# Optimization experiments

Measured on AMD Instinct MI355X. Metric: run time of the kernel, lower is better.

Reference implementation:

```python
import jax, jax.numpy as jnp
import numpy as np

NUM_COMPONENTS = 4
HEADS = 24
DIM_HEAD = 64
EPS = 1e-8

def setup_inputs() -> dict:
    key = jax.random.key(0)
    ks = jax.random.split(key, 6)
    BC, S, D = 8, 4096, 1536   # batch*components, spatial tokens, hidden dim
    T = 154                     # encoder (text) sequence length
    w_scale = D ** -0.5
    return {
        "hidden_states": jax.random.normal(ks[0], (BC, S, D), jnp.float32),
        "encoder_hidden_states": jax.random.normal(ks[1], (BC, T, D), jnp.float32),
        "Wq": jax.random.normal(ks[2], (D, D), jnp.float32) * w_scale,
        "bq": jnp.zeros((D,), jnp.float32),
        "Wk": jax.random.normal(ks[3], (D, D), jnp.float32) * w_scale,
        "bk": jnp.zeros((D,), jnp.float32),
        "Wv": jax.random.normal(ks[4], (D, D), jnp.float32) * w_scale,
        "bv": jnp.zeros((D,), jnp.float32),
        "Wo": jax.random.normal(ks[5], (D, D), jnp.float32) * w_scale,
        "bo": jnp.zeros((D,), jnp.float32),
    }

def reference(hidden_states, encoder_hidden_states, Wq, bq, Wk, bk, Wv, bv, Wo, bo):
    BC, S, D = hidden_states.shape
    T = encoder_hidden_states.shape[1]
    C = NUM_COMPONENTS
    B = BC // C
    H, dh = HEADS, DIM_HEAD
    scale = dh ** -0.5

    # linear projections (torch Linear: x @ W.T + b)
    q = hidden_states @ Wq.T + bq            # [BC, S, D]
    k = encoder_hidden_states @ Wk.T + bk     # [BC, T, D]
    v = encoder_hidden_states @ Wv.T + bv     # [BC, T, D]

    q = q.reshape(BC, S, H, dh).transpose(0, 2, 1, 3)  # [BC, H, S, dh]
    k = k.reshape(BC, T, H, dh).transpose(0, 2, 1, 3)  # [BC, H, T, dh]
    v = v.reshape(BC, T, H, dh).transpose(0, 2, 1, 3)  # [BC, H, T, dh]

    # full score tensor, softmax over the COMPONENT axis, then renormalize over keys
    scores = jnp.einsum('bhsd,bhtd->bhst', q, k) * scale        # [BC, H, S, T]
    scores = scores.reshape(C, B, H, S, T)
    w = jax.nn.softmax(scores, axis=0).reshape(BC, H, S, T)
    w = w / (jnp.sum(w, axis=-1, keepdims=True) + EPS)

    out = jnp.einsum('bhst,bhtd->bhsd', w, v)                   # [BC, H, S, dh]
    out = out.transpose(0, 2, 1, 3).reshape(BC, S, D)
    out = out @ Wo.T + bo
    return out
```

## Files before the change

kernel.cpp:

```cpp
#include <hip/hip_runtime.h>


typedef unsigned short u16;
typedef unsigned int   u32;

#define NHS   50331648ULL
#define NEHS  1892352ULL
#define NW    2359296ULL
#define NVT   1966080ULL

using bf16x8 = __attribute__((ext_vector_type(8))) short;
using f32x4  = __attribute__((ext_vector_type(4))) float;

__device__ __forceinline__ u16 f2bf(float f) {
  union { float f; u32 u; } x{f};
  u32 r = (x.u + 0x7fffu + ((x.u >> 16) & 1u)) >> 16;
  return (u16)r;
}

__device__ __forceinline__ void gload_lds16(const u16* g, u16* s) {
  __builtin_amdgcn_global_load_lds((const __attribute__((address_space(1))) void*)g,
                                   (__attribute__((address_space(3))) void*)s,
                                   16, 0, 0);
}

__global__ void cvt_bf16(const float* __restrict__ src, u16* __restrict__ dst, int n4) {
  int idx = blockIdx.x * blockDim.x + threadIdx.x;
  int stride = gridDim.x * blockDim.x;
  for (int i = idx; i < n4; i += stride) {
    float4 v = ((const float4*)src)[i];
    ushort4 o;
    o.x = f2bf(v.x); o.y = f2bf(v.y); o.z = f2bf(v.z); o.w = f2bf(v.w);
    ((ushort4*)dst)[i] = o;
  }
}

template <int MODE>
__global__ __launch_bounds__(256)
void gemm_bt(const u16* __restrict__ A, const u16* __restrict__ Bw,
             const float* __restrict__ bias, void* __restrict__ Cv,
             int M, int K) {
  const int N = 1536;
  __shared__ __align__(16) u16 As[4096];
  __shared__ __align__(16) u16 Bs[4096];
  const int tid  = threadIdx.x;
  const int wv   = tid >> 6;
  const int lane = tid & 63;
  const int wr = wv >> 1, wc = wv & 1;
  const int l16 = lane & 15, quad = lane >> 4;
  const int m0 = blockIdx.y * 128, n0 = blockIdx.x * 128;
  const int r = tid >> 2, c8 = (tid & 3) * 8;

  int ra0 = m0 + r;      if (ra0 > M - 1) ra0 = M - 1;
  int ra1 = m0 + 64 + r; if (ra1 > M - 1) ra1 = M - 1;
  const u16* a0 = A  + (size_t)ra0 * K + c8;
  const u16* a1 = A  + (size_t)ra1 * K + c8;
  const u16* b0 = Bw + (size_t)(n0 + r) * K + c8;
  const u16* b1 = Bw + (size_t)(n0 + 64 + r) * K + c8;
  u16* asd0 = &As[tid * 8];
  u16* asd1 = &As[2048 + tid * 8];
  u16* bsd0 = &Bs[tid * 8];
  u16* bsd1 = &Bs[2048 + tid * 8];

  f32x4 acc[4][4];
#pragma unroll
  for (int i = 0; i < 4; ++i)
#pragma unroll
    for (int j = 0; j < 4; ++j) acc[i][j] = {0.f, 0.f, 0.f, 0.f};

  for (int kt = 0; kt < K; kt += 32) {
    __syncthreads();
    gload_lds16(a0 + kt, asd0);
    gload_lds16(a1 + kt, asd1);
    gload_lds16(b0 + kt, bsd0);
    gload_lds16(b1 + kt, bsd1);
    __syncthreads();
    bf16x8 af[4], bfr[4];
#pragma unroll
    for (int i = 0; i < 4; ++i) {
      af[i]  = *(const bf16x8*)&As[(wr * 64 + i * 16 + l16) * 32 + quad * 8];
      bfr[i] = *(const bf16x8*)&Bs[(wc * 64 + i * 16 + l16) * 32 + quad * 8];
    }
#pragma unroll
    for (int i = 0; i < 4; ++i)
#pragma unroll
      for (int j = 0; j < 4; ++j)
        acc[i][j] = __builtin_amdgcn_mfma_f32_16x16x32_bf16(af[i], bfr[j], acc[i][j], 0, 0, 0);
  }

#pragma unroll
  for (int i = 0; i < 4; ++i) {
    const int rb = m0 + wr * 64 + i * 16 + quad * 4;
#pragma unroll
    for (int j = 0; j < 4; ++j) {
      const int col = n0 + wc * 64 + j * 16 + l16;
      const float bvs = bias[col];
#pragma unroll
      for (int rr = 0; rr < 4; ++rr) {
        const int row = rb + rr;
        if (row < M) {
          float v = acc[i][j][rr] + bvs;
          if (MODE == 0) {
            ((float*)Cv)[(size_t)row * N + col] = v;
          } else if (MODE == 1) {
            ((u16*)Cv)[(size_t)row * N + col] = f2bf(v);
          } else {
            const int bc = row / 154;
            const int t  = row - bc * 154;
            ((u16*)Cv)[((size_t)bc * 1536 + col) * 160 + t] = f2bf(v);
          }
        }
      }
    }
  }
}

__global__ __launch_bounds__(256, 2)
void attn_kernel(const u16* __restrict__ qg, const u16* __restrict__ kg,
                 const u16* __restrict__ vtg, u16* __restrict__ og) {
  __shared__ __align__(16) u16 lds[40960];

  const int tid  = threadIdx.x;
  const int wv   = tid >> 6;
  const int lane = tid & 63;
  const int l16 = lane & 15, quad = lane >> 4;
  const int s0 = blockIdx.x * 64;
  const int h  = blockIdx.y;
  const int b  = blockIdx.z;
  const int swz = ((quad ^ ((l16 >> 1) & 3)) * 8);

  {
    const u16* kbase = kg + (size_t)b * 154 * 1536 + h * 64;
#pragma unroll
    for (int p = 0; p < 20; ++p) {
      const int L = p * 256 + tid;
      const int r = L >> 2;
      const int t = r % 160;
      const int cks = r / 160;
      const int c = cks >> 1, ks = cks & 1;
      const int csrc = ((L & 3) ^ ((t >> 1) & 3)) * 8;
      const u16* src = kbase + ((size_t)c * 308 + t) * 1536 + ks * 32 + csrc;
      gload_lds16(src, &lds[(size_t)L * 8]);
    }
  }

  bf16x8 qa[4][2];
#pragma unroll
  for (int c = 0; c < 4; ++c) {
    const u16* qrow = qg + ((size_t)((c * 2 + b) * 4096 + s0 + wv * 16 + l16)) * 1536 + h * 64;
#pragma unroll
    for (int ks = 0; ks < 2; ++ks)
      qa[c][ks] = *(const bf16x8*)(qrow + ks * 32 + quad * 8);
  }
  __syncthreads();

  f32x4 sc[4][10];
#pragma unroll
  for (int c = 0; c < 4; ++c)
#pragma unroll
    for (int nt = 0; nt < 10; ++nt) sc[c][nt] = {0.f, 0.f, 0.f, 0.f};

#pragma unroll
  for (int nt = 0; nt < 10; ++nt)
#pragma unroll
    for (int c = 0; c < 4; ++c)
#pragma unroll
      for (int ks = 0; ks < 2; ++ks) {
        bf16x8 kf = *(const bf16x8*)&lds[((c * 2 + ks) * 160 + nt * 16 + l16) * 32 + swz];
        sc[c][nt] = __builtin_amdgcn_mfma_f32_16x16x32_bf16(qa[c][ks], kf, sc[c][nt], 0, 0, 0);
      }

  float rs[4][4];
#pragma unroll
  for (int c = 0; c < 4; ++c)
#pragma unroll
    for (int rr = 0; rr < 4; ++rr) rs[c][rr] = 0.f;

#pragma unroll
  for (int nt = 0; nt < 10; ++nt) {
    const int t = nt * 16 + l16;
    const bool ok = (t < 154);
#pragma unroll
    for (int rr = 0; rr < 4; ++rr) {
      float v0 = sc[0][nt][rr] * 0.125f;
      float v1 = sc[1][nt][rr] * 0.125f;
      float v2 = sc[2][nt][rr] * 0.125f;
      float v3 = sc[3][nt][rr] * 0.125f;
      float m = fmaxf(fmaxf(v0, v1), fmaxf(v2, v3));
      float e0 = __expf(v0 - m), e1 = __expf(v1 - m);
      float e2 = __expf(v2 - m), e3 = __expf(v3 - m);
      float inv = 1.f / (e0 + e1 + e2 + e3);
      float w0 = ok ? e0 * inv : 0.f;
      float w1 = ok ? e1 * inv : 0.f;
      float w2 = ok ? e2 * inv : 0.f;
      float w3 = ok ? e3 * inv : 0.f;
      sc[0][nt][rr] = w0; sc[1][nt][rr] = w1; sc[2][nt][rr] = w2; sc[3][nt][rr] = w3;
      rs[0][rr] += w0; rs[1][rr] += w1; rs[2][rr] += w2; rs[3][rr] += w3;
    }
  }
#pragma unroll
  for (int c = 0; c < 4; ++c)
#pragma unroll
    for (int rr = 0; rr < 4; ++rr) {
      float v = rs[c][rr];
      v += __shfl_xor(v, 1); v += __shfl_xor(v, 2);
      v += __shfl_xor(v, 4); v += __shfl_xor(v, 8);
      rs[c][rr] = 1.f / (v + 1e-8f);
    }

  __syncthreads();

  const u16* vbase = vtg + ((size_t)b * 1536 + h * 64) * 160;

  auto stage_v = [&](int c, int par) {
    const u16* vb = vbase + (size_t)c * 2 * 1536 * 160;
    u16* slot = &lds[20480 + par * 10240];
#pragma unroll
    for (int p = 0; p < 5; ++p) {
      const int L = p * 256 + tid;
      const int row = L >> 2;
      const int ks = row >> 6, dh = row & 63;
      const int csrc = ((L & 3) ^ ((dh >> 1) & 3)) * 8;
      gload_lds16(vb + dh * 160 + ks * 32 + csrc, &slot[(size_t)L * 8]);
    }
  };

  auto write_w = [&](int c, int par) {
    u16* slot = &lds[par * 10240];
#pragma unroll
    for (int nt = 0; nt < 10; ++nt) {
#pragma unroll
      for (int rr = 0; rr < 4; ++rr) {
        const int srow = wv * 16 + quad * 4 + rr;
        const int t = nt * 16 + l16;
        const int cl = ((t >> 3) & 3) ^ ((srow >> 1) & 3);
        slot[srow * 160 + (t >> 5) * 32 + cl * 8 + (t & 7)] =
            f2bf(sc[c][nt][rr] * rs[c][rr]);
      }
    }
  };

  f32x4 oacc[4][4];
#pragma unroll
  for (int c = 0; c < 4; ++c)
#pragma unroll
    for (int nd = 0; nd < 4; ++nd) oacc[c][nd] = {0.f, 0.f, 0.f, 0.f};

  stage_v(0, 0);
  write_w(0, 0);
#pragma unroll
  for (int c = 0; c < 4; ++c) {
    __syncthreads();
    if (c < 3) { stage_v(c + 1, (c + 1) & 1); write_w(c + 1, (c + 1) & 1); }
    const int par = c & 1;
    const u16* sw = &lds[par * 10240];
    const u16* sv = &lds[20480 + par * 10240];
#pragma unroll
    for (int ks = 0; ks < 5; ++ks) {
      bf16x8 wa = *(const bf16x8*)&sw[(wv * 16 + l16) * 160 + ks * 32 + swz];
#pragma unroll
      for (int nd = 0; nd < 4; ++nd) {
        bf16x8 vf = *(const bf16x8*)&sv[(ks * 64 + nd * 16 + l16) * 32 + swz];
        oacc[c][nd] = __builtin_amdgcn_mfma_f32_16x16x32_bf16(wa, vf, oacc[c][nd], 0, 0, 0);
      }
    }
  }

#pragma unroll
  for (int c = 0; c < 4; ++c)
#pragma unroll
    for (int nd = 0; nd < 4; ++nd)
#pragma unroll
      for (int rr = 0; rr < 4; ++rr) {
        const int srow = s0 + wv * 16 + quad * 4 + rr;
        og[((size_t)((c * 2 + b) * 4096 + srow)) * 1536 + h * 64 + nd * 16 + l16] =
            f2bf(oacc[c][nd][rr]);
      }
}

extern "C" void kernel_launch(void* const* d_in, const int* in_sizes, int n_in,
                              void* d_out, int out_size, void* d_ws, size_t ws_size,
                              hipStream_t stream) {
  (void)in_sizes; (void)n_in; (void)out_size; (void)ws_size;
  const float* hs  = (const float*)d_in[0];
  const float* ehs = (const float*)d_in[1];
  const float* Wq  = (const float*)d_in[2];
  const float* bq  = (const float*)d_in[3];
  const float* Wk  = (const float*)d_in[4];
  const float* bk  = (const float*)d_in[5];
  const float* Wv  = (const float*)d_in[6];
  const float* bv  = (const float*)d_in[7];
  const float* Wo  = (const float*)d_in[8];
  const float* bo  = (const float*)d_in[9];
  float* out = (float*)d_out;

  u16* ws   = (u16*)d_ws;
  u16* hsb  = ws;
  u16* ehsb = hsb + NHS;
  u16* wqb  = ehsb + NEHS;
  u16* wkb  = wqb + NW;
  u16* wvb  = wkb + NW;
  u16* wob  = wvb + NW;
  u16* qb   = wob + NW;
  u16* kgb  = qb + NHS;
  u16* vtb  = kgb + NEHS;
  u16* atb  = vtb + NVT;

  auto cvt = [&](const float* s, u16* d, size_t n) {
    int n4 = (int)(n / 4);
    int blocks = (n4 + 255) / 256;
    if (blocks > 8192) blocks = 8192;
    cvt_bf16<<<blocks, 256, 0, stream>>>(s, d, n4);
  };
  cvt(hs, hsb, NHS);
  cvt(ehs, ehsb, NEHS);
  cvt(Wq, wqb, NW);
  cvt(Wk, wkb, NW);
  cvt(Wv, wvb, NW);
  cvt(Wo, wob, NW);

  gemm_bt<1><<<dim3(12, 256), 256, 0, stream>>>(hsb, wqb, bq, qb, 32768, 1536);
  gemm_bt<1><<<dim3(12, 10),  256, 0, stream>>>(ehsb, wkb, bk, kgb, 1232, 1536);
  gemm_bt<2><<<dim3(12, 10),  256, 0, stream>>>(ehsb, wvb, bv, vtb, 1232, 1536);

  attn_kernel<<<dim3(64, 24, 2), 256, 0, stream>>>(qb, kgb, vtb, atb);

  gemm_bt<0><<<dim3(12, 256), 256, 0, stream>>>(atb, wob, bo, out, 32768, 1536);
}
```

Measured before the change: 1.057 ms.

## Add 256x256-tile pipelined GEMM for the large Q and output projections

Adds a specialised 512-thread GEMM kernel for the two large projections (32768x1536x1536). It uses 256x256 output tiles, a 4-deep LDS ring filled by direct global-to-LDS loads with an XOR swizzle, and a remapped block order that groups tiles for better L2 reuse. Each wave computes a 128x64 sub-tile and raises its priority around the MFMA loop. The aim is more data reuse per byte loaded and overlap of loads with compute, at the cost of high register and LDS use (128 KB LDS, 128 accumulator floats per thread), which can limit occupancy.

```diff
diff --git a/kernel.cpp b/kernel.cpp
--- a/kernel.cpp
+++ b/kernel.cpp
@@ -23,6 +23,8 @@
                                    (__attribute__((address_space(3))) void*)s,
                                    16, 0, 0);
 }
+
+#define WAITV(N) asm volatile("s_waitcnt vmcnt(" #N ")" ::: "memory")
 
 __global__ void cvt_bf16(const float* __restrict__ src, u16* __restrict__ dst, int n4) {
   int idx = blockIdx.x * blockDim.x + threadIdx.x;
@@ -32,6 +34,110 @@
     ushort4 o;
     o.x = f2bf(v.x); o.y = f2bf(v.y); o.z = f2bf(v.z); o.w = f2bf(v.w);
     ((ushort4*)dst)[i] = o;
+  }
+}
+
+template <int MODE>
+__global__ __launch_bounds__(512, 2)
+void gemm_big(const u16* __restrict__ Ag, const u16* __restrict__ Bw,
+              const float* __restrict__ bias, void* __restrict__ Cv) {
+  __shared__ __align__(16) u16 lds[65536];
+
+  const int tid  = threadIdx.x;
+  const int wv   = tid >> 6;
+  const int lane = tid & 63;
+  const int l16  = lane & 15, quad = lane >> 4;
+  const int wm = wv >> 2, wn = wv & 3;
+
+  const int wg = ((int)blockIdx.x & 7) * 96 + ((int)blockIdx.x >> 3);
+  const int by = wg & 127;
+  const int bx = wg >> 7;
+  const int m0 = by * 256, n0 = bx * 256;
+
+  const u16* gsrc[4];
+  int ldst[4];
+#pragma unroll
+  for (int q = 0; q < 4; ++q) {
+    const int L = q * 512 + tid;
+    const int cid = L & 1023;
+    const int row = cid >> 2;
+    const int csrc = ((L & 3) ^ ((row >> 1) & 3)) * 8;
+    gsrc[q] = (L < 1024 ? Ag + (size_t)(m0 + row) * 1536
+                        : Bw + (size_t)(n0 + row) * 1536) + csrc;
+    ldst[q] = L * 8;
+  }
+
+  int aoff[8], boff[4];
+#pragma unroll
+  for (int i = 0; i < 8; ++i) {
+    const int ra = wm * 128 + i * 16 + l16;
+    aoff[i] = ra * 32 + ((quad ^ ((ra >> 1) & 3)) * 8);
+  }
+#pragma unroll
+  for (int j = 0; j < 4; ++j) {
+    const int rb = wn * 64 + j * 16 + l16;
+    boff[j] = 8192 + rb * 32 + ((quad ^ ((rb >> 1) & 3)) * 8);
+  }
+
+  f32x4 acc[8][4];
+#pragma unroll
+  for (int i = 0; i < 8; ++i)
+#pragma unroll
+    for (int j = 0; j < 4; ++j) acc[i][j] = {0.f, 0.f, 0.f, 0.f};
+
+  auto stage = [&](int tile) {
+    u16* dst = &lds[(tile & 3) * 16384];
+    const int kt = tile * 32;
+#pragma unroll
+    for (int q = 0; q < 4; ++q)
+      gload_lds16(gsrc[q] + kt, dst + ldst[q]);
+  };
+
+  auto compute = [&](int tile) {
+    const u16* buf = &lds[(tile & 3) * 16384];
+    __builtin_amdgcn_s_setprio(1);
+    bf16x8 bfr[4];
+#pragma unroll
+    for (int j = 0; j < 4; ++j) bfr[j] = *(const bf16x8*)&buf[boff[j]];
+#pragma unroll
+    for (int i = 0; i < 8; ++i) {
+      bf16x8 af = *(const bf16x8*)&buf[aoff[i]];
+#pragma unroll
+      for (int j = 0; j < 4; ++j)
+        acc[i][j] = __builtin_amdgcn_mfma_f32_16x16x32_bf16(af, bfr[j], acc[i][j], 0, 0, 0);
+    }
+    __builtin_amdgcn_s_setprio(0);
+  };
+
+  stage(0); stage(1); stage(2);
+  WAITV(8);
+  __builtin_amdgcn_s_barrier();
+
+  for (int t = 0; t < 45; ++t) {
+    stage(t + 3);
+    compute(t);
+    WAITV(8);
+    __builtin_amdgcn_s_barrier();
+  }
+  compute(45); WAITV(4); __builtin_amdgcn_s_barrier();
+  compute(46); WAITV(0); __builtin_amdgcn_s_barrier();
+  compute(47);
+
+#pragma unroll
+  for (int i = 0; i < 8; ++i) {
+    const int row0 = m0 + wm * 128 + i * 16 + quad * 4;
+#pragma unroll
+    for (int j = 0; j < 4; ++j) {
+      const int col = n0 + wn * 64 + j * 16 + l16;
+      const float bvs = bias[col];
+#pragma unroll
+      for (int rr = 0; rr < 4; ++rr) {
+        const int row = row0 + rr;
+        const float v = acc[i][j][rr] + bvs;
+        if (MODE == 0) ((float*)Cv)[(size_t)row * 1536 + col] = v;
+        else           ((u16*)Cv)[(size_t)row * 1536 + col] = f2bf(v);
+      }
+    }
   }
 }
 
@@ -100,9 +206,7 @@
         const int row = rb + rr;
         if (row < M) {
           float v = acc[i][j][rr] + bvs;
-          if (MODE == 0) {
-            ((float*)Cv)[(size_t)row * N + col] = v;
-          } else if (MODE == 1) {
+          if (MODE == 1) {
             ((u16*)Cv)[(size_t)row * N + col] = f2bf(v);
           } else {
             const int bc = row / 154;
@@ -319,11 +423,11 @@
   cvt(Wv, wvb, NW);
   cvt(Wo, wob, NW);
 
-  gemm_bt<1><<<dim3(12, 256), 256, 0, stream>>>(hsb, wqb, bq, qb, 32768, 1536);
-  gemm_bt<1><<<dim3(12, 10),  256, 0, stream>>>(ehsb, wkb, bk, kgb, 1232, 1536);
-  gemm_bt<2><<<dim3(12, 10),  256, 0, stream>>>(ehsb, wvb, bv, vtb, 1232, 1536);
+  gemm_big<1><<<dim3(768), 512, 0, stream>>>(hsb, wqb, bq, qb);
+  gemm_bt<1><<<dim3(12, 10), 256, 0, stream>>>(ehsb, wkb, bk, kgb, 1232, 1536);
+  gemm_bt<2><<<dim3(12, 10), 256, 0, stream>>>(ehsb, wvb, bv, vtb, 1232, 1536);
 
   attn_kernel<<<dim3(64, 24, 2), 256, 0, stream>>>(qb, kgb, vtb, atb);
 
-  gemm_bt<0><<<dim3(12, 256), 256, 0, stream>>>(atb, wob, bo, out, 32768, 1536);
-}
+  gemm_big<0><<<dim3(768), 512, 0, stream>>>(atb, wob, bo, out);
+}
```

Result: faster. 909.4 us (-14.0%).
